# Kernel tuning notes

Measured on AMD Instinct MI355X. Metric: run time of the kernel, lower is better.

The kernel has to match this reference:

```python
import jax, jax.numpy as jnp
import numpy as np

N_OBS = 2_097_152
N_BAND = 4
T_SPAN = 3650.0  # days


def setup_inputs() -> dict:
    key = jax.random.key(0)
    k0, k1, k2, k3, k4, k5 = jax.random.split(key, 6)
    t = jnp.sort(jax.random.uniform(k0, (N_OBS,), jnp.float32) * T_SPAN)
    band = jax.random.randint(k1, (N_OBS,), 0, N_BAND)
    y = jax.random.normal(k2, (N_OBS,), jnp.float32)
    yerr = 0.1 + 0.9 * jax.random.uniform(k3, (N_OBS,), jnp.float32)
    log_amp_delta = 0.1 * jax.random.normal(k4, (N_BAND - 1,), jnp.float32)
    # [log sigma, log ell] for the quasisep Exp kernel
    log_kernel_param = jnp.array([0.0, np.log(50.0)], dtype=jnp.float32) + \
        0.1 * jax.random.normal(k5, (2,), jnp.float32)
    return {"t": t, "band": band, "y": y, "yerr": yerr,
            "log_amp_delta": log_amp_delta, "log_kernel_param": log_kernel_param}


def _log_prob(t, band, y, yerr, log_amp_delta, log_kernel_param):
    # amp_transform: prepend 0 -> per-band amplitudes
    amps = jnp.exp(jnp.concatenate([jnp.zeros(1, log_amp_delta.dtype), log_amp_delta]))
    sigma2 = jnp.exp(2.0 * log_kernel_param[0])
    ell = jnp.exp(log_kernel_param[1])

    # lag_transform with zero lags: sort by time (assume_sorted path of tinygp)
    inds = jnp.argsort(t)
    ts, b = t[inds], band[inds]
    ys, dg = y[inds], (yerr ** 2)[inds]

    # multiband Exp kernel: K_ij = sigma2 * u_i * u_j * exp(-(t_i - t_j)/ell), i>=j
    u = amps[b]                       # per-point amplitude
    a = dg + sigma2 * u * u           # diagonal K_ii + noise
    U = sigma2 * u                    # semiseparable left factor
    V = u                             # semiseparable right factor
    dt = jnp.diff(ts)
    P = jnp.concatenate([jnp.zeros(1, ts.dtype), jnp.exp(-dt / ell)])  # decay factors

    # Celerite O(N) Cholesky (K = L D L^T) fused with the forward solve L z = y.
    def step(carry, x):
        cS, cg = carry                # cS = S_{n-1} + D_{n-1} W_{n-1}^2 ; cg = g_{n-1} + W_{n-1} z_{n-1}
        Pn, an, Un, Vn, yn = x
        Sn = Pn * Pn * cS
        gn = Pn * cg
        Dn = an - Un * Un * Sn
        Wn = (Vn - Sn * Un) / Dn
        zn = yn - Un * gn
        return (Sn + Dn * Wn * Wn, gn + Wn * zn), (jnp.log(Dn), zn * zn / Dn)

    zero = jnp.zeros((), ts.dtype)
    _, (logD, quad) = jax.lax.scan(step, (zero, zero), (P, a, U, V, ys))
    n = ts.shape[0]
    return -0.5 * (jnp.sum(quad) + jnp.sum(logD) + n * jnp.log(2.0 * jnp.pi))


def reference(t, band, y, yerr, log_amp_delta, log_kernel_param):
    return _log_prob(t, band, y, yerr, log_amp_delta, log_kernel_param)
```

## Files before the change

### kernel.cpp

```cpp
#include <hip/hip_runtime.h>
#include <math.h>

#define N_TOTAL 2097152
#define NT 256
#define NC 16
#define EPB (NT * NC)
#define NB (N_TOTAL / EPB)

struct DMat { double al, be, ga, de, c, e, f; };

__device__ __forceinline__ DMat dmat_identity() {
    DMat m; m.al = 1.0; m.be = 0.0; m.ga = 0.0; m.de = 1.0; m.c = 1.0; m.e = 0.0; m.f = 0.0;
    return m;
}

__device__ __forceinline__ DMat dmat_compose(const DMat& A, const DMat& B) {
    DMat r;
    r.al = A.al * B.al + A.be * B.ga;
    r.be = A.al * B.be + A.be * B.de;
    r.ga = A.ga * B.al + A.de * B.ga;
    r.de = A.ga * B.be + A.de * B.de;
    r.c  = A.c * B.c;
    r.e  = A.e * B.al + A.c * B.e + A.f * B.ga;
    r.f  = A.e * B.be + A.c * B.f + A.f * B.de;
    return r;
}

__device__ __forceinline__ void dmat_normalize(DMat& m) {
    double mx = fmax(fabs(m.al), fabs(m.be));
    mx = fmax(mx, fabs(m.ga));
    mx = fmax(mx, fabs(m.de));
    mx = fmax(mx, fabs(m.c));
    mx = fmax(mx, fabs(m.e));
    mx = fmax(mx, fabs(m.f));
    if (!(mx > 0.0) || isinf(mx)) return;
    double inv = 1.0 / mx;
    m.al *= inv; m.be *= inv; m.ga *= inv; m.de *= inv;
    m.c *= inv; m.e *= inv; m.f *= inv;
}

__device__ __forceinline__ void dmat_store(double* sm, int i, const DMat& m) {
    sm[0 * NT + i] = m.al; sm[1 * NT + i] = m.be; sm[2 * NT + i] = m.ga;
    sm[3 * NT + i] = m.de; sm[4 * NT + i] = m.c;  sm[5 * NT + i] = m.e;
    sm[6 * NT + i] = m.f;
}

__device__ __forceinline__ DMat dmat_load(const double* sm, int i) {
    DMat m;
    m.al = sm[0 * NT + i]; m.be = sm[1 * NT + i]; m.ga = sm[2 * NT + i];
    m.de = sm[3 * NT + i]; m.c  = sm[4 * NT + i]; m.e  = sm[5 * NT + i];
    m.f  = sm[6 * NT + i];
    return m;
}

__device__ __forceinline__ DMat dmat_scan_inclusive(double* sm, DMat mine, int tid) {
    dmat_store(sm, tid, mine);
    __syncthreads();
    for (int d = 1; d < NT; d <<= 1) {
        DMat o;
        bool has = (tid >= d);
        if (has) o = dmat_load(sm, tid - d);
        __syncthreads();
        if (has) {
            mine = dmat_compose(mine, o);
            dmat_normalize(mine);
            dmat_store(sm, tid, mine);
        }
        __syncthreads();
    }
    return mine;
}

__device__ __forceinline__ DMat elem_mat(double P, double a, double U, double V, double yy) {
    double p = P * P;
    DMat m;
    m.al = p * (a - 2.0 * U * V);
    m.be = V * V;
    m.ga = -(p * U * U);
    m.de = a;
    m.c  = P * (a - U * V);
    m.e  = -(yy * p * U);
    m.f  = yy * V;
    return m;
}

__global__ __launch_bounds__(NT) void k_upsweep(
    const float* __restrict__ t, const int* __restrict__ band,
    const float* __restrict__ y, const float* __restrict__ yerr,
    const float* __restrict__ lad, const float* __restrict__ lkp,
    double* __restrict__ block_comp)
{
    __shared__ double sm[7 * NT];
    const int tid = threadIdx.x;
    const double sigma2 = exp(2.0 * (double)lkp[0]);
    const double inv_ell = exp(-(double)lkp[1]);
    double amps[4];
    amps[0] = 1.0;
    amps[1] = exp((double)lad[0]);
    amps[2] = exp((double)lad[1]);
    amps[3] = exp((double)lad[2]);

    const int base = (blockIdx.x * NT + tid) * NC;
    double tprev = (base == 0) ? 0.0 : (double)t[base - 1];
    DMat acc = dmat_identity();
    #pragma unroll
    for (int k = 0; k < NC; k += 4) {
        float4 tv = *reinterpret_cast<const float4*>(t + base + k);
        float4 yv = *reinterpret_cast<const float4*>(y + base + k);
        float4 ev = *reinterpret_cast<const float4*>(yerr + base + k);
        int4   bv = *reinterpret_cast<const int4*>(band + base + k);
        float tc[4] = {tv.x, tv.y, tv.z, tv.w};
        float yc[4] = {yv.x, yv.y, yv.z, yv.w};
        float ec[4] = {ev.x, ev.y, ev.z, ev.w};
        int   bc[4] = {bv.x, bv.y, bv.z, bv.w};
        #pragma unroll
        for (int j = 0; j < 4; ++j) {
            double u = amps[bc[j] & 3];
            double a = (double)ec[j] * (double)ec[j] + sigma2 * u * u;
            double U = sigma2 * u;
            double P = ((base + k + j) == 0) ? 0.0
                     : exp(-((double)tc[j] - tprev) * inv_ell);
            acc = dmat_compose(elem_mat(P, a, U, u, (double)yc[j]), acc);
            tprev = (double)tc[j];
        }
    }
    dmat_normalize(acc);
    DMat incl = dmat_scan_inclusive(sm, acc, tid);
    if (tid == NT - 1) {
        double* o = block_comp + blockIdx.x * 7;
        o[0] = incl.al; o[1] = incl.be; o[2] = incl.ga; o[3] = incl.de;
        o[4] = incl.c;  o[5] = incl.e;  o[6] = incl.f;
    }
}

__global__ __launch_bounds__(NT) void k_spine(
    const double* __restrict__ block_comp, double* __restrict__ block_excl)
{
    __shared__ double sm[7 * NT];
    const int tid = threadIdx.x;
    const double* p0 = block_comp + (2 * tid) * 7;
    const double* p1 = block_comp + (2 * tid + 1) * 7;
    DMat m0 = {p0[0], p0[1], p0[2], p0[3], p0[4], p0[5], p0[6]};
    DMat m1 = {p1[0], p1[1], p1[2], p1[3], p1[4], p1[5], p1[6]};
    DMat mine = dmat_compose(m1, m0);
    dmat_normalize(mine);
    dmat_scan_inclusive(sm, mine, tid);
    DMat E = (tid == 0) ? dmat_identity() : dmat_load(sm, tid - 1);
    double* o0 = block_excl + (2 * tid) * 7;
    o0[0] = E.al; o0[1] = E.be; o0[2] = E.ga; o0[3] = E.de;
    o0[4] = E.c;  o0[5] = E.e;  o0[6] = E.f;
    DMat M = dmat_compose(m0, E);
    dmat_normalize(M);
    double* o1 = block_excl + (2 * tid + 1) * 7;
    o1[0] = M.al; o1[1] = M.be; o1[2] = M.ga; o1[3] = M.de;
    o1[4] = M.c;  o1[5] = M.e;  o1[6] = M.f;
}

__global__ __launch_bounds__(NT) void k_replay(
    const float* __restrict__ t, const int* __restrict__ band,
    const float* __restrict__ y, const float* __restrict__ yerr,
    const float* __restrict__ lad, const float* __restrict__ lkp,
    const double* __restrict__ block_excl, double* __restrict__ accum)
{
    __shared__ double sm[7 * NT];
    const int tid = threadIdx.x;
    const double sigma2 = exp(2.0 * (double)lkp[0]);
    const double inv_ell = exp(-(double)lkp[1]);
    double amps[4];
    amps[0] = 1.0;
    amps[1] = exp((double)lad[0]);
    amps[2] = exp((double)lad[1]);
    amps[3] = exp((double)lad[2]);

    const int base = (blockIdx.x * NT + tid) * NC;
    double tprev = (base == 0) ? 0.0 : (double)t[base - 1];

    double Pv[NC];
    float av[NC], Uv[NC], Vv[NC], yv_[NC];
    DMat acc = dmat_identity();
    #pragma unroll
    for (int k = 0; k < NC; k += 4) {
        float4 tv = *reinterpret_cast<const float4*>(t + base + k);
        float4 yv = *reinterpret_cast<const float4*>(y + base + k);
        float4 ev = *reinterpret_cast<const float4*>(yerr + base + k);
        int4   bv = *reinterpret_cast<const int4*>(band + base + k);
        float tc[4] = {tv.x, tv.y, tv.z, tv.w};
        float yc[4] = {yv.x, yv.y, yv.z, yv.w};
        float ec[4] = {ev.x, ev.y, ev.z, ev.w};
        int   bc[4] = {bv.x, bv.y, bv.z, bv.w};
        #pragma unroll
        for (int j = 0; j < 4; ++j) {
            double u = amps[bc[j] & 3];
            double a = (double)ec[j] * (double)ec[j] + sigma2 * u * u;
            double U = sigma2 * u;
            double P = ((base + k + j) == 0) ? 0.0
                     : exp(-((double)tc[j] - tprev) * inv_ell);
            Pv[k + j] = P;
            av[k + j] = (float)a; Uv[k + j] = (float)U;
            Vv[k + j] = (float)u; yv_[k + j] = yc[j];
            acc = dmat_compose(elem_mat(P, a, U, u, (double)yc[j]), acc);
            tprev = (double)tc[j];
        }
    }
    dmat_normalize(acc);
    dmat_scan_inclusive(sm, acc, tid);
    DMat E = (tid == 0) ? dmat_identity() : dmat_load(sm, tid - 1);

    const double* pb = block_excl + blockIdx.x * 7;
    DMat Eb = {pb[0], pb[1], pb[2], pb[3], pb[4], pb[5], pb[6]};
    DMat F = dmat_compose(E, Eb);
    dmat_normalize(F);
    double x = 0.0, g = 0.0;
    if (F.de != 0.0 && !isinf(F.de)) {
        double invde = 1.0 / F.de;
        x = F.be * invde;
        g = F.f  * invde;
    }
    if (!isfinite(x)) x = 0.0;
    if (!isfinite(g)) g = 0.0;

    double s_logD = 0.0, s_quad = 0.0;
    #pragma unroll
    for (int k = 0; k < NC; ++k) {
        double P = Pv[k], a = (double)av[k], U = (double)Uv[k];
        double V = (double)Vv[k], yy = (double)yv_[k];
        double p = P * P;
        double S = p * x;
        double D = a - U * U * S;
        if (!(D > 1e-300)) D = 1e-300;
        double W = (V - S * U) / D;
        double gn = P * g;
        double z = yy - U * gn;
        s_logD += log(D);
        s_quad += z * z / D;
        x = S + D * W * W;
        g = gn + W * z;
    }

    __syncthreads();
    sm[tid] = s_logD;
    sm[NT + tid] = s_quad;
    __syncthreads();
    for (int d = NT / 2; d > 0; d >>= 1) {
        if (tid < d) {
            sm[tid] += sm[tid + d];
            sm[NT + tid] += sm[NT + tid + d];
        }
        __syncthreads();
    }
    if (tid == 0) {
        atomicAdd(&accum[0], sm[0]);
        atomicAdd(&accum[1], sm[NT]);
    }
}

__global__ void k_zero(double* __restrict__ accum) {
    accum[0] = 0.0;
    accum[1] = 0.0;
}

__global__ void k_final(const double* __restrict__ accum, float* __restrict__ out) {
    double r = -0.5 * (accum[0] + accum[1]
                       + (double)N_TOTAL * 1.8378770664093454836);
    out[0] = (float)r;
}

extern "C" void kernel_launch(void* const* d_in, const int* in_sizes, int n_in,
                              void* d_out, int out_size, void* d_ws, size_t ws_size,
                              hipStream_t stream)
{
    const float* t    = (const float*)d_in[0];
    const int*   band = (const int*)d_in[1];
    const float* y    = (const float*)d_in[2];
    const float* yerr = (const float*)d_in[3];
    const float* lad  = (const float*)d_in[4];
    const float* lkp  = (const float*)d_in[5];

    double* dws        = (double*)d_ws;
    double* block_comp = dws;
    double* block_excl = dws + NB * 7;
    double* accum      = dws + 2 * NB * 7;

    k_zero<<<1, 1, 0, stream>>>(accum);
    k_upsweep<<<NB, NT, 0, stream>>>(t, band, y, yerr, lad, lkp, block_comp);
    k_spine<<<1, NT, 0, stream>>>(block_comp, block_excl);
    k_replay<<<NB, NT, 0, stream>>>(t, band, y, yerr, lad, lkp, block_excl, accum);
    k_final<<<1, 1, 0, stream>>>(accum, (float*)d_out);
}
```

Baseline: 124.1 us.

## Compute element matrices and serial replay in fp32, fold zero/final kernels

Element-matrix construction, the decay exponentials and the per-element sequential Cholesky replay now run in single precision with fast intrinsics (__expf, __logf) instead of double. The block-level composition and scan stay in double. The separate zero and final kernels are removed: the spine kernel zeroes the accumulators and a counter, and the last replay block computes the output. The aim is to cut FP64 arithmetic and two kernel launches, at the cost of reduced numerical accuracy over long recurrences and a dropped normalization of F.

```diff
diff --git a/kernel.cpp b/kernel.cpp
--- a/kernel.cpp
+++ b/kernel.cpp
@@ -71,16 +71,18 @@
     return mine;
 }
 
-__device__ __forceinline__ DMat elem_mat(double P, double a, double U, double V, double yy) {
-    double p = P * P;
+__device__ __forceinline__ DMat elem_mat_f32(float P, float dg, float s2u2,
+                                             float sigma2, float u, float yy) {
+    float p = P * P;
+    float U = sigma2 * u;
     DMat m;
-    m.al = p * (a - 2.0 * U * V);
-    m.be = V * V;
-    m.ga = -(p * U * U);
-    m.de = a;
-    m.c  = P * (a - U * V);
-    m.e  = -(yy * p * U);
-    m.f  = yy * V;
+    m.al = (double)(p * (dg - s2u2));
+    m.be = (double)(u * u);
+    m.ga = -(double)(p * U * U);
+    m.de = (double)(dg + s2u2);
+    m.c  = (double)(P * dg);
+    m.e  = -(double)(yy * p * U);
+    m.f  = (double)(yy * u);
     return m;
 }
 
@@ -92,16 +94,16 @@
 {
     __shared__ double sm[7 * NT];
     const int tid = threadIdx.x;
-    const double sigma2 = exp(2.0 * (double)lkp[0]);
-    const double inv_ell = exp(-(double)lkp[1]);
-    double amps[4];
-    amps[0] = 1.0;
-    amps[1] = exp((double)lad[0]);
-    amps[2] = exp((double)lad[1]);
-    amps[3] = exp((double)lad[2]);
+    const float sigma2 = __expf(2.f * lkp[0]);
+    const float inv_ell = __expf(-lkp[1]);
+    float amps[4];
+    amps[0] = 1.f;
+    amps[1] = __expf(lad[0]);
+    amps[2] = __expf(lad[1]);
+    amps[3] = __expf(lad[2]);
 
     const int base = (blockIdx.x * NT + tid) * NC;
-    double tprev = (base == 0) ? 0.0 : (double)t[base - 1];
+    float tprev = (base == 0) ? 0.f : t[base - 1];
     DMat acc = dmat_identity();
     #pragma unroll
     for (int k = 0; k < NC; k += 4) {
@@ -115,13 +117,13 @@
         int   bc[4] = {bv.x, bv.y, bv.z, bv.w};
         #pragma unroll
         for (int j = 0; j < 4; ++j) {
-            double u = amps[bc[j] & 3];
-            double a = (double)ec[j] * (double)ec[j] + sigma2 * u * u;
-            double U = sigma2 * u;
-            double P = ((base + k + j) == 0) ? 0.0
-                     : exp(-((double)tc[j] - tprev) * inv_ell);
-            acc = dmat_compose(elem_mat(P, a, U, u, (double)yc[j]), acc);
-            tprev = (double)tc[j];
+            float u = amps[bc[j] & 3];
+            float dg = ec[j] * ec[j];
+            float s2u2 = sigma2 * u * u;
+            float P = ((base + k + j) == 0) ? 0.f
+                    : __expf(-(tc[j] - tprev) * inv_ell);
+            acc = dmat_compose(elem_mat_f32(P, dg, s2u2, sigma2, u, yc[j]), acc);
+            tprev = tc[j];
         }
     }
     dmat_normalize(acc);
@@ -134,10 +136,16 @@
 }
 
 __global__ __launch_bounds__(NT) void k_spine(
-    const double* __restrict__ block_comp, double* __restrict__ block_excl)
+    const double* __restrict__ block_comp, double* __restrict__ block_excl,
+    double* __restrict__ accum, unsigned int* __restrict__ counter)
 {
     __shared__ double sm[7 * NT];
     const int tid = threadIdx.x;
+    if (tid == 0) {
+        accum[0] = 0.0;
+        accum[1] = 0.0;
+        *counter = 0u;
+    }
     const double* p0 = block_comp + (2 * tid) * 7;
     const double* p1 = block_comp + (2 * tid + 1) * 7;
     DMat m0 = {p0[0], p0[1], p0[2], p0[3], p0[4], p0[5], p0[6]};
@@ -160,23 +168,23 @@
     const float* __restrict__ t, const int* __restrict__ band,
     const float* __restrict__ y, const float* __restrict__ yerr,
     const float* __restrict__ lad, const float* __restrict__ lkp,
-    const double* __restrict__ block_excl, double* __restrict__ accum)
+    const double* __restrict__ block_excl, double* __restrict__ accum,
+    unsigned int* __restrict__ counter, float* __restrict__ out)
 {
     __shared__ double sm[7 * NT];
     const int tid = threadIdx.x;
-    const double sigma2 = exp(2.0 * (double)lkp[0]);
-    const double inv_ell = exp(-(double)lkp[1]);
-    double amps[4];
-    amps[0] = 1.0;
-    amps[1] = exp((double)lad[0]);
-    amps[2] = exp((double)lad[1]);
-    amps[3] = exp((double)lad[2]);
+    const float sigma2 = __expf(2.f * lkp[0]);
+    const float inv_ell = __expf(-lkp[1]);
+    float amps[4];
+    amps[0] = 1.f;
+    amps[1] = __expf(lad[0]);
+    amps[2] = __expf(lad[1]);
+    amps[3] = __expf(lad[2]);
 
     const int base = (blockIdx.x * NT + tid) * NC;
-    double tprev = (base == 0) ? 0.0 : (double)t[base - 1];
-
-    double Pv[NC];
-    float av[NC], Uv[NC], Vv[NC], yv_[NC];
+    float tprev = (base == 0) ? 0.f : t[base - 1];
+
+    float Pv[NC], dgv[NC], uv[NC], yv_[NC];
     DMat acc = dmat_identity();
     #pragma unroll
     for (int k = 0; k < NC; k += 4) {
@@ -190,16 +198,14 @@
         int   bc[4] = {bv.x, bv.y, bv.z, bv.w};
         #pragma unroll
         for (int j = 0; j < 4; ++j) {
-            double u = amps[bc[j] & 3];
-            double a = (double)ec[j] * (double)ec[j] + sigma2 * u * u;
-            double U = sigma2 * u;
-            double P = ((base + k + j) == 0) ? 0.0
-                     : exp(-((double)tc[j] - tprev) * inv_ell);
-            Pv[k + j] = P;
-            av[k + j] = (float)a; Uv[k + j] = (float)U;
-            Vv[k + j] = (float)u; yv_[k + j] = yc[j];
-            acc = dmat_compose(elem_mat(P, a, U, u, (double)yc[j]), acc);
-            tprev = (double)tc[j];
+            float u = amps[bc[j] & 3];
+            float dg = ec[j] * ec[j];
+            float s2u2 = sigma2 * u * u;
+            float P = ((base + k + j) == 0) ? 0.f
+                    : __expf(-(tc[j] - tprev) * inv_ell);
+            Pv[k + j] = P; dgv[k + j] = dg; uv[k + j] = u; yv_[k + j] = yc[j];
+            acc = dmat_compose(elem_mat_f32(P, dg, s2u2, sigma2, u, yc[j]), acc);
+            tprev = tc[j];
         }
     }
     dmat_normalize(acc);
@@ -209,37 +215,37 @@
     const double* pb = block_excl + blockIdx.x * 7;
     DMat Eb = {pb[0], pb[1], pb[2], pb[3], pb[4], pb[5], pb[6]};
     DMat F = dmat_compose(E, Eb);
-    dmat_normalize(F);
-    double x = 0.0, g = 0.0;
-    if (F.de != 0.0 && !isinf(F.de)) {
+    float x = 0.f, g = 0.f;
+    if (F.de != 0.0) {
         double invde = 1.0 / F.de;
-        x = F.be * invde;
-        g = F.f  * invde;
-    }
-    if (!isfinite(x)) x = 0.0;
-    if (!isfinite(g)) g = 0.0;
-
-    double s_logD = 0.0, s_quad = 0.0;
+        x = (float)(F.be * invde);
+        g = (float)(F.f  * invde);
+    }
+    if (!isfinite(x)) x = 0.f;
+    if (!isfinite(g)) g = 0.f;
+
+    float s_logD = 0.f, s_quad = 0.f;
     #pragma unroll
     for (int k = 0; k < NC; ++k) {
-        double P = Pv[k], a = (double)av[k], U = (double)Uv[k];
-        double V = (double)Vv[k], yy = (double)yv_[k];
-        double p = P * P;
-        double S = p * x;
-        double D = a - U * U * S;
-        if (!(D > 1e-300)) D = 1e-300;
-        double W = (V - S * U) / D;
-        double gn = P * g;
-        double z = yy - U * gn;
-        s_logD += log(D);
+        float P = Pv[k], dg = dgv[k], u = uv[k], yy = yv_[k];
+        float U = sigma2 * u;
+        float a = dg + U * u;
+        float p = P * P;
+        float S = p * x;
+        float D = a - U * U * S;
+        if (!(D > 1e-30f)) D = 1e-30f;
+        float W = (u - S * U) / D;
+        float gn = P * g;
+        float z = yy - U * gn;
+        s_logD += __logf(D);
         s_quad += z * z / D;
         x = S + D * W * W;
         g = gn + W * z;
     }
 
     __syncthreads();
-    sm[tid] = s_logD;
-    sm[NT + tid] = s_quad;
+    sm[tid] = (double)s_logD;
+    sm[NT + tid] = (double)s_quad;
     __syncthreads();
     for (int d = NT / 2; d > 0; d >>= 1) {
         if (tid < d) {
@@ -251,18 +257,16 @@
     if (tid == 0) {
         atomicAdd(&accum[0], sm[0]);
         atomicAdd(&accum[1], sm[NT]);
-    }
-}
-
-__global__ void k_zero(double* __restrict__ accum) {
-    accum[0] = 0.0;
-    accum[1] = 0.0;
-}
-
-__global__ void k_final(const double* __restrict__ accum, float* __restrict__ out) {
-    double r = -0.5 * (accum[0] + accum[1]
+        __threadfence();
+        unsigned int old = atomicAdd(counter, 1u);
+        if (old == NB - 1) {
+            double s0 = atomicAdd(&accum[0], 0.0);
+            double s1 = atomicAdd(&accum[1], 0.0);
+            double r = -0.5 * (s0 + s1
                        + (double)N_TOTAL * 1.8378770664093454836);
-    out[0] = (float)r;
+            out[0] = (float)r;
+        }
+    }
 }
 
 extern "C" void kernel_launch(void* const* d_in, const int* in_sizes, int n_in,
@@ -280,10 +284,10 @@
     double* block_comp = dws;
     double* block_excl = dws + NB * 7;
     double* accum      = dws + 2 * NB * 7;
-
-    k_zero<<<1, 1, 0, stream>>>(accum);
+    unsigned int* counter = (unsigned int*)(accum + 2);
+
     k_upsweep<<<NB, NT, 0, stream>>>(t, band, y, yerr, lad, lkp, block_comp);
-    k_spine<<<1, NT, 0, stream>>>(block_comp, block_excl);
-    k_replay<<<NB, NT, 0, stream>>>(t, band, y, yerr, lad, lkp, block_excl, accum);
-    k_final<<<1, 1, 0, stream>>>(accum, (float*)d_out);
-}
+    k_spine<<<1, NT, 0, stream>>>(block_comp, block_excl, accum, counter);
+    k_replay<<<NB, NT, 0, stream>>>(t, band, y, yerr, lad, lkp, block_excl,
+                                    accum, counter, (float*)d_out);
+}
```

Result: no change. 126.5 us (+1.9%).
